# Kernel tuning notes

Hardware: AMD Instinct MI355X
Metric: run time of the kernel (lower is better)

The kernel has to match this reference:

```python
import jax, jax.numpy as jnp
import numpy as np

B, S, E = 8, 1024, 768
H, D = 12, 64
SCALE = 1.0 / np.sqrt(D).astype(np.float32)


def setup_inputs() -> dict:
    key = jax.random.key(0)
    ks = jax.random.split(key, 12)
    s = 0.02
    inp = {
        "queries": jax.random.normal(ks[0], (B, S, E), jnp.float32),
        "keys": jax.random.normal(ks[1], (B, S, E), jnp.float32),
        "values": jax.random.normal(ks[2], (B, S, E), jnp.float32),
        # causal mask for decoder attention (True = keep)
        "attn_mask": jnp.tril(jnp.ones((S, S), dtype=bool)),
        # per-head projections stacked over the head axis
        "Wq": jax.random.normal(ks[3], (H, E, D), jnp.float32) * s,
        "bq": jax.random.normal(ks[4], (H, D), jnp.float32) * s,
        "Wk": jax.random.normal(ks[5], (H, E, D), jnp.float32) * s,
        "bk": jax.random.normal(ks[6], (H, D), jnp.float32) * s,
        "Wv": jax.random.normal(ks[7], (H, E, D), jnp.float32) * s,
        "bv": jax.random.normal(ks[8], (H, D), jnp.float32) * s,
        "Wo": jax.random.normal(ks[9], (H * D, E), jnp.float32) * s,
        "bo": jax.random.normal(ks[10], (E,), jnp.float32) * s,
    }
    return inp


def reference(queries, keys, values, attn_mask, Wq, bq, Wk, bk, Wv, bv, Wo, bo):
    # Batched equivalent of the per-head Python loop (eval mode: dropout is identity).
    Q = jnp.einsum("bse,hed->bhsd", queries, Wq) + bq[:, None, :]   # [B,H,S,D]
    K = jnp.einsum("bte,hed->bhtd", keys, Wk) + bk[:, None, :]
    V = jnp.einsum("bte,hed->bhtd", values, Wv) + bv[:, None, :]
    scores = jnp.einsum("bhsd,bhtd->bhst", Q, K) * SCALE             # [B,H,S,S]
    scores = jnp.where(attn_mask, scores, -jnp.inf)
    weights = jax.nn.softmax(scores, axis=-1)
    heads = jnp.einsum("bhst,bhtd->bhsd", weights, V)                # [B,H,S,D]
    concat = heads.transpose(0, 2, 1, 3).reshape(queries.shape[0], queries.shape[1], -1)  # [B,S,H*D]
    return concat @ Wo + bo                                          # [B,S,E]
```

## Files before the change

kernel.cpp:

```cpp
#include <hip/hip_runtime.h>

#define B_ 8
#define S_ 1024
#define E_ 768
#define H_ 12
#define D_ 64
#define HD_ 768
#define SCALE_ 0.125f

typedef short s16x8 __attribute__((ext_vector_type(8)));
typedef float f32x4 __attribute__((ext_vector_type(4)));
typedef unsigned int u32x4 __attribute__((ext_vector_type(4)));
typedef unsigned short u16;
typedef unsigned int u32;

#define MFMA16(a,b,c) __builtin_amdgcn_mfma_f32_16x16x32_bf16((a),(b),(c),0,0,0)

__device__ __forceinline__ u16 f2bf(float x){
  unsigned u = __float_as_uint(x);
  u += 0x7fffu + ((u >> 16) & 1u);
  return (u16)(u >> 16);
}

__device__ __forceinline__ u32 pack2(float a, float b){
  return (u32)f2bf(a) | ((u32)f2bf(b) << 16);
}

__device__ __forceinline__ u32 cvtpk(float a, float b){
  u32 r;
  asm("v_cvt_pk_bf16_f32 %0, %1, %2" : "=v"(r) : "v"(a), "v"(b));
  return r;
}

#define GLOAD_LDS16(srcp, dstp)                                                        \
  __builtin_amdgcn_global_load_lds(                                                    \
      (const __attribute__((address_space(1))) u32*)(srcp),                            \
      (__attribute__((address_space(3))) u32*)(dstp), 16, 0, 0)

__global__ void prep_weights(const float* __restrict__ Wq, const float* __restrict__ Wk,
                             const float* __restrict__ Wv, const float* __restrict__ Wo,
                             u16* __restrict__ Wt_qkv, u16* __restrict__ Wot) {
  __shared__ float t[64][65];
  const int bid = blockIdx.x;
  const int tid = threadIdx.x;
  const int c = tid & 63;
  const int rg = tid >> 6;
  if (bid < 432) {
    int z = bid / 144, r = bid % 144, h = r / 12, et = r % 12;
    const float* W = (z == 0) ? Wq : ((z == 1) ? Wk : Wv);
    const float* src = W + (size_t)(h * E_ + et * 64) * D_;
#pragma unroll
    for (int p = 0; p < 16; ++p)
      t[rg + 4 * p][c] = src[(rg + 4 * p) * D_ + c];
    __syncthreads();
    u16* dst = Wt_qkv + (size_t)z * HD_ * E_ + (h * 64) * E_ + et * 64;
#pragma unroll
    for (int p = 0; p < 16; ++p) {
      int d = rg + 4 * p;
      dst[d * E_ + c] = f2bf(t[c][d]);
    }
  } else {
    int r = bid - 432; int kt = r / 12, nt = r % 12;
    const float* src = Wo + (size_t)(kt * 64) * E_ + nt * 64;
#pragma unroll
    for (int p = 0; p < 16; ++p)
      t[rg + 4 * p][c] = src[(rg + 4 * p) * E_ + c];
    __syncthreads();
    u16* dst = Wot + (size_t)(nt * 64) * HD_ + kt * 64;
#pragma unroll
    for (int p = 0; p < 16; ++p) {
      int nl = rg + 4 * p;
      dst[nl * HD_ + c] = f2bf(t[c][nl]);
    }
  }
}

__launch_bounds__(256)
__global__ void qkv_gemm(const float* __restrict__ qin, const float* __restrict__ kin,
                         const float* __restrict__ vin, const u16* __restrict__ Wt_qkv,
                         const float* __restrict__ bq, const float* __restrict__ bk,
                         const float* __restrict__ bv, u16* __restrict__ Qbf,
                         u16* __restrict__ Kbf, u16* __restrict__ Vt) {
  __shared__ __align__(16) float Asf[128 * 64];
  __shared__ __align__(16) u16  Bs[128 * 64];
  const int tid = threadIdx.x;
  const int lane = tid & 63;
  const int w = tid >> 6;
  const int wr = w >> 1, wc = w & 1;
  const int m0 = blockIdx.x * 128;
  const int n0 = blockIdx.y * 128;
  const int z  = blockIdx.z;
  const float* in = (z == 0) ? qin : ((z == 1) ? kin : vin);
  const u16* Wt = Wt_qkv + z * (HD_ * E_);
  const float* bias = (z == 0) ? bq : ((z == 1) ? bk : bv);

  f32x4 acc[4][4];
#pragma unroll
  for (int i = 0; i < 4; ++i)
#pragma unroll
    for (int j = 0; j < 4; ++j) acc[i][j] = (f32x4){0.f, 0.f, 0.f, 0.f};

  const int g = lane >> 4;
  const int l15 = lane & 15;
  const int arow = lane >> 4;
  const int ach  = lane & 15;
  const int brow = lane >> 3;
  const int bch  = lane & 7;

  for (int kt = 0; kt < E_ / 64; ++kt) {
    __syncthreads();
#pragma unroll
    for (int i = 0; i < 8; ++i) {
      int row = i * 16 + w * 4 + arow;
      GLOAD_LDS16(in + (size_t)(m0 + row) * E_ + kt * 64 + ((ach ^ (row & 15)) << 2),
                  &Asf[(i * 16 + w * 4) * 64]);
    }
#pragma unroll
    for (int j = 0; j < 4; ++j) {
      int row = j * 32 + w * 8 + brow;
      GLOAD_LDS16(Wt + (n0 + row) * E_ + kt * 64 + ((bch ^ (row & 7)) << 3),
                  &Bs[(j * 32 + w * 8) * 64]);
    }
    __syncthreads();
#pragma unroll
    for (int kk = 0; kk < 2; ++kk) {
      const int kc = kk * 4 + g;
      s16x8 af[4], bfr[4];
#pragma unroll
      for (int i = 0; i < 4; ++i) {
        int row = wr * 64 + i * 16 + l15;
        const float* rp = Asf + row * 64;
        f32x4 lo = *(const f32x4*)(rp + ((( 2 * kc )     ^ (row & 15)) << 2));
        f32x4 hi = *(const f32x4*)(rp + ((( 2 * kc + 1 ) ^ (row & 15)) << 2));
        u32x4 q;
        q[0] = cvtpk(lo[0], lo[1]);
        q[1] = cvtpk(lo[2], lo[3]);
        q[2] = cvtpk(hi[0], hi[1]);
        q[3] = cvtpk(hi[2], hi[3]);
        af[i] = __builtin_bit_cast(s16x8, q);
      }
#pragma unroll
      for (int j = 0; j < 4; ++j) {
        int row = wc * 64 + j * 16 + l15;
        bfr[j] = *(const s16x8*)(Bs + row * 64 + ((kc ^ (row & 7)) << 3));
      }
#pragma unroll
      for (int i = 0; i < 4; ++i)
#pragma unroll
        for (int j = 0; j < 4; ++j) acc[i][j] = MFMA16(af[i], bfr[j], acc[i][j]);
    }
  }
#pragma unroll
  for (int j = 0; j < 4; ++j) {
    int ng = n0 + wc * 64 + j * 16 + l15;
    float bvv = bias[ng];
    int h = ng >> 6, d = ng & 63;
#pragma unroll
    for (int i = 0; i < 4; ++i) {
#pragma unroll
      for (int r = 0; r < 4; ++r) {
        int m = m0 + wr * 64 + i * 16 + g * 4 + r;
        float v = acc[i][j][r] + bvv;
        int bb = m >> 10, s = m & 1023;
        if (z == 0) {
          v *= SCALE_;
          Qbf[((bb * H_ + h) * S_ + s) * D_ + d] = f2bf(v);
        } else if (z == 1) {
          Kbf[((bb * H_ + h) * S_ + s) * D_ + d] = f2bf(v);
        } else {
          Vt[((bb * H_ + h) * D_ + d) * S_ + s] = f2bf(v);
        }
      }
    }
  }
}

__launch_bounds__(256)
__global__ void attn_kernel(const u16* __restrict__ Qbf, const u16* __restrict__ Kbf,
                            const u16* __restrict__ Vt, u16* __restrict__ concat) {
  __shared__ __align__(16) u16 Ks[2][64 * 64];
  __shared__ __align__(16) u16 Vs[2][64 * 64];
  __shared__ __align__(16) u16 Ps[4][2][16 * 64];
  const int tid = threadIdx.x;
  const int lane = tid & 63;
  const int w = tid >> 6;
  const int l15 = lane & 15;
  const int g = lane >> 4;
  const int qb = blockIdx.x & 7;
  const int bh = blockIdx.x >> 3;
  const int h = bh % H_;
  const int b = bh / H_;
  const u16* Qb = Qbf + (b * H_ + h) * S_ * D_;
  const u16* Kb = Kbf + (b * H_ + h) * S_ * D_;
  const u16* Vb = Vt  + (b * H_ + h) * D_ * S_;
  const int q0 = qb * 128;
  const int qrow_base = q0 + w * 32;

  s16x8 qf[2][2];
#pragma unroll
  for (int qg = 0; qg < 2; ++qg)
#pragma unroll
    for (int kk = 0; kk < 2; ++kk)
      qf[qg][kk] = *(const s16x8*)(Qb + (qrow_base + qg * 16 + l15) * D_ + kk * 32 + g * 8);

  f32x4 o[2][4];
#pragma unroll
  for (int qg = 0; qg < 2; ++qg)
#pragma unroll
    for (int dc = 0; dc < 4; ++dc) o[qg][dc] = (f32x4){0.f, 0.f, 0.f, 0.f};
  float lsum[2] = {0.f, 0.f};

  const int nt = 2 * qb + 2;
  const int srow = lane >> 3;
  const int schunk = lane & 7;

#define STAGE(tt, bsel)                                                              \
  {                                                                                  \
    const int t0s = (tt) * 64;                                                       \
    _Pragma("unroll")                                                                \
    for (int j = 0; j < 2; ++j) {                                                    \
      int row = w * 16 + j * 8 + srow;                                               \
      GLOAD_LDS16(Kb + (t0s + row) * D_ + ((schunk ^ (row & 7)) << 3),               \
                  &Ks[bsel][(w * 16 + j * 8) * 64]);                                 \
      GLOAD_LDS16(Vb + row * S_ + t0s + ((schunk ^ (row & 7)) << 3),                 \
                  &Vs[bsel][(w * 16 + j * 8) * 64]);                                 \
    }                                                                                \
  }

  STAGE(0, 0);
  __syncthreads();
  int cur = 0;
  for (int t = 0; t < nt; ++t) {
    if (t + 1 < nt) STAGE(t + 1, cur ^ 1);
    const int t0 = t * 64;
    const u16* Kl = Ks[cur];
    const u16* Vl = Vs[cur];
    f32x4 st[2][4];
#pragma unroll
    for (int qg = 0; qg < 2; ++qg)
#pragma unroll
      for (int c = 0; c < 4; ++c) st[qg][c] = (f32x4){0.f, 0.f, 0.f, 0.f};
#pragma unroll
    for (int kk = 0; kk < 2; ++kk) {
      s16x8 kf[4];
#pragma unroll
      for (int c = 0; c < 4; ++c) {
        int row = 16 * c + l15;
        kf[c] = *(const s16x8*)(Kl + row * 64 + ((((kk << 2) + g) ^ (row & 7)) << 3));
      }
#pragma unroll
      for (int qg = 0; qg < 2; ++qg)
#pragma unroll
        for (int c = 0; c < 4; ++c) st[qg][c] = MFMA16(kf[c], qf[qg][kk], st[qg][c]);
    }
#pragma unroll
    for (int qg = 0; qg < 2; ++qg) {
      const int qmin = qrow_base + qg * 16;
      if (t0 > qmin + 15) continue;
      const bool needmask = (t0 + 63 > qmin);
      const int qv = qmin + l15;
      u16* Pq = Ps[w][qg];
      float lacc = 0.f;
#pragma unroll
      for (int c = 0; c < 4; ++c) {
        float p[4];
#pragma unroll
        for (int r = 0; r < 4; ++r) {
          float s = st[qg][c][r];
          if (needmask && (t0 + 16 * c + 4 * g + r > qv)) s = -1e30f;
          p[r] = __expf(s);
          lacc += p[r];
        }
        int chunk = (2 * c + (g >> 1)) ^ (l15 & 7);
        *(uint2*)(Pq + l15 * 64 + (chunk << 3) + ((g & 1) << 2)) =
            make_uint2(pack2(p[0], p[1]), pack2(p[2], p[3]));
      }
      lsum[qg] += lacc;
    }
    asm volatile("s_waitcnt lgkmcnt(0)" ::: "memory");
    __builtin_amdgcn_sched_barrier(0);
#pragma unroll
    for (int kk = 0; kk < 2; ++kk) {
      s16x8 vf[4];
#pragma unroll
      for (int dc = 0; dc < 4; ++dc) {
        int row = 16 * dc + l15;
        vf[dc] = *(const s16x8*)(Vl + row * 64 + ((((kk << 2) + g) ^ (row & 7)) << 3));
      }
#pragma unroll
      for (int qg = 0; qg < 2; ++qg) {
        if (t0 > qrow_base + qg * 16 + 15) continue;
        s16x8 pf = *(const s16x8*)(Ps[w][qg] + l15 * 64 +
                                   ((((kk << 2) + g) ^ (l15 & 7)) << 3));
#pragma unroll
        for (int dc = 0; dc < 4; ++dc) o[qg][dc] = MFMA16(vf[dc], pf, o[qg][dc]);
      }
    }
    __syncthreads();
    cur ^= 1;
  }
#pragma unroll
  for (int qg = 0; qg < 2; ++qg) {
    float l = lsum[qg];
    l += __shfl_xor(l, 16);
    l += __shfl_xor(l, 32);
    float linv = 1.0f / l;
    int q = qrow_base + qg * 16 + l15;
    u16* Cr = concat + (b * S_ + q) * HD_ + h * D_;
#pragma unroll
    for (int dc = 0; dc < 4; ++dc) {
      *(uint2*)(Cr + dc * 16 + g * 4) =
          make_uint2(pack2(o[qg][dc][0] * linv, o[qg][dc][1] * linv),
                     pack2(o[qg][dc][2] * linv, o[qg][dc][3] * linv));
    }
  }
#undef STAGE
}

__launch_bounds__(256)
__global__ void out_gemm(const u16* __restrict__ concat, const u16* __restrict__ Wot,
                         const float* __restrict__ bo, float* __restrict__ out) {
  __shared__ __align__(16) u16 As[128 * 64];
  __shared__ __align__(16) u16 Bs[128 * 64];
  const int tid = threadIdx.x;
  const int lane = tid & 63;
  const int w = tid >> 6;
  const int wr = w >> 1, wc = w & 1;
  const int m0 = blockIdx.x * 128;
  const int n0 = blockIdx.y * 128;
  f32x4 acc[4][4];
#pragma unroll
  for (int i = 0; i < 4; ++i)
#pragma unroll
    for (int j = 0; j < 4; ++j) acc[i][j] = (f32x4){0.f, 0.f, 0.f, 0.f};
  const int g = lane >> 4;
  const int l15 = lane & 15;
  const int srow = lane >> 3;
  const int sch  = (lane & 7) ^ srow;

  for (int kt = 0; kt < HD_ / 64; ++kt) {
    __syncthreads();
#pragma unroll
    for (int i = 0; i < 4; ++i) {
      int row = i * 32 + w * 8 + srow;
      GLOAD_LDS16(concat + (m0 + row) * HD_ + kt * 64 + sch * 8, &As[(i * 32 + w * 8) * 64]);
      GLOAD_LDS16(Wot    + (n0 + row) * HD_ + kt * 64 + sch * 8, &Bs[(i * 32 + w * 8) * 64]);
    }
    __syncthreads();
#pragma unroll
    for (int kk = 0; kk < 2; ++kk) {
      const int kc = kk * 4 + g;
      s16x8 af[4], bfr[4];
#pragma unroll
      for (int i = 0; i < 4; ++i) {
        int row = wr * 64 + i * 16 + l15;
        af[i] = *(const s16x8*)(As + row * 64 + ((kc ^ (row & 7)) << 3));
      }
#pragma unroll
      for (int j = 0; j < 4; ++j) {
        int row = wc * 64 + j * 16 + l15;
        bfr[j] = *(const s16x8*)(Bs + row * 64 + ((kc ^ (row & 7)) << 3));
      }
#pragma unroll
      for (int i = 0; i < 4; ++i)
#pragma unroll
        for (int j = 0; j < 4; ++j) acc[i][j] = MFMA16(af[i], bfr[j], acc[i][j]);
    }
  }
#pragma unroll
  for (int j = 0; j < 4; ++j) {
    int ng = n0 + wc * 64 + j * 16 + l15;
    float bvv = bo[ng];
#pragma unroll
    for (int i = 0; i < 4; ++i) {
      int mrow = m0 + wr * 64 + i * 16 + g * 4;
#pragma unroll
      for (int r = 0; r < 4; ++r) out[(mrow + r) * E_ + ng] = acc[i][j][r] + bvv;
    }
  }
}

extern "C" void kernel_launch(void* const* d_in, const int* in_sizes, int n_in,
                              void* d_out, int out_size, void* d_ws, size_t ws_size,
                              hipStream_t stream) {
  const float* queries = (const float*)d_in[0];
  const float* keys    = (const float*)d_in[1];
  const float* values  = (const float*)d_in[2];
  const float* Wq = (const float*)d_in[4];
  const float* bq = (const float*)d_in[5];
  const float* Wk = (const float*)d_in[6];
  const float* bk = (const float*)d_in[7];
  const float* Wv = (const float*)d_in[8];
  const float* bv = (const float*)d_in[9];
  const float* Wo = (const float*)d_in[10];
  const float* bo = (const float*)d_in[11];
  float* out = (float*)d_out;

  u16* Wt_qkv = (u16*)d_ws;
  u16* Wot    = Wt_qkv + 3 * HD_ * E_;
  u16* Qbf    = Wot + E_ * HD_;
  u16* Kbf    = Qbf + B_ * H_ * S_ * D_;
  u16* Vt     = Kbf + B_ * H_ * S_ * D_;
  u16* concat = Vt  + B_ * H_ * S_ * D_;

  prep_weights<<<dim3(576), dim3(256), 0, stream>>>(Wq, Wk, Wv, Wo, Wt_qkv, Wot);
  qkv_gemm<<<dim3(64, 6, 3), dim3(256), 0, stream>>>(
      queries, keys, values, Wt_qkv, bq, bk, bv, Qbf, Kbf, Vt);
  attn_kernel<<<dim3(768), dim3(256), 0, stream>>>(Qbf, Kbf, Vt, concat);
  out_gemm<<<dim3(64, 6), dim3(256), 0, stream>>>(concat, Wot, bo, out);
}
```

Measured before the change: 147.8 us.

## Double-buffer QKV GEMM LDS tiles with K=32 stages and async prefetch

Restructures the QKV projection GEMM main loop to use two LDS buffers of K=32 slices. The global-to-LDS load for stage t+2 is issued while stage t is computed, using vmcnt waits and raw barriers in place of full __syncthreads. MFMA priority is raised with s_setprio. This aims to hide global load latency behind matrix math. The cost is more barriers per K and smaller per-stage work, with swizzle patterns rewritten for the 32-wide rows.

```diff
diff --git a/kernel.cpp b/kernel.cpp
--- a/kernel.cpp
+++ b/kernel.cpp
@@ -81,8 +81,8 @@
                          const float* __restrict__ bq, const float* __restrict__ bk,
                          const float* __restrict__ bv, u16* __restrict__ Qbf,
                          u16* __restrict__ Kbf, u16* __restrict__ Vt) {
-  __shared__ __align__(16) float Asf[128 * 64];
-  __shared__ __align__(16) u16  Bs[128 * 64];
+  __shared__ __align__(16) float Asf[2][128 * 32];
+  __shared__ __align__(16) u16  Bs[2][128 * 32];
   const int tid = threadIdx.x;
   const int lane = tid & 63;
   const int w = tid >> 6;
@@ -102,54 +102,76 @@
 
   const int g = lane >> 4;
   const int l15 = lane & 15;
-  const int arow = lane >> 4;
-  const int ach  = lane & 15;
-  const int brow = lane >> 3;
-  const int bch  = lane & 7;
-
-  for (int kt = 0; kt < E_ / 64; ++kt) {
-    __syncthreads();
-#pragma unroll
-    for (int i = 0; i < 8; ++i) {
-      int row = i * 16 + w * 4 + arow;
-      GLOAD_LDS16(in + (size_t)(m0 + row) * E_ + kt * 64 + ((ach ^ (row & 15)) << 2),
-                  &Asf[(i * 16 + w * 4) * 64]);
+  const int aro = lane >> 3;
+  const int schA = (lane & 7) ^ aro;
+  const int bro = lane >> 2;
+  const int schB = (lane & 3) ^ (bro & 3);
+
+#define QSTAGE(kt, bsel)                                                              \
+  {                                                                                   \
+    _Pragma("unroll")                                                                 \
+    for (int i = 0; i < 4; ++i) {                                                     \
+      int row = i * 32 + w * 8 + aro;                                                 \
+      GLOAD_LDS16(in + (size_t)(m0 + row) * E_ + (kt) * 32 + schA * 4,                \
+                  &Asf[bsel][(i * 32 + w * 8) * 32]);                                 \
+    }                                                                                 \
+    _Pragma("unroll")                                                                 \
+    for (int j = 0; j < 2; ++j) {                                                     \
+      int row = j * 64 + w * 16 + bro;                                                \
+      GLOAD_LDS16(Wt + (n0 + row) * E_ + (kt) * 32 + schB * 8,                        \
+                  &Bs[bsel][(j * 64 + w * 16) * 32]);                                 \
+    }                                                                                 \
+  }
+
+  QSTAGE(0, 0);
+  QSTAGE(1, 1);
+  asm volatile("s_waitcnt vmcnt(6)" ::: "memory");
+  __builtin_amdgcn_sched_barrier(0);
+  __builtin_amdgcn_s_barrier();
+  __builtin_amdgcn_sched_barrier(0);
+  for (int t = 0; t < 24; ++t) {
+    const int cur = t & 1;
+    const float* Al = Asf[cur];
+    const u16*   Bl = Bs[cur];
+    s16x8 af[4], bfr[4];
+#pragma unroll
+    for (int i = 0; i < 4; ++i) {
+      int row = wr * 64 + i * 16 + l15;
+      const float* rp = Al + row * 32;
+      f32x4 lo = *(const f32x4*)(rp + (((2 * g)     ^ (row & 7)) << 2));
+      f32x4 hi = *(const f32x4*)(rp + (((2 * g + 1) ^ (row & 7)) << 2));
+      u32x4 q;
+      q[0] = cvtpk(lo[0], lo[1]);
+      q[1] = cvtpk(lo[2], lo[3]);
+      q[2] = cvtpk(hi[0], hi[1]);
+      q[3] = cvtpk(hi[2], hi[3]);
+      af[i] = __builtin_bit_cast(s16x8, q);
     }
 #pragma unroll
     for (int j = 0; j < 4; ++j) {
-      int row = j * 32 + w * 8 + brow;
-      GLOAD_LDS16(Wt + (n0 + row) * E_ + kt * 64 + ((bch ^ (row & 7)) << 3),
-                  &Bs[(j * 32 + w * 8) * 64]);
-    }
-    __syncthreads();
-#pragma unroll
-    for (int kk = 0; kk < 2; ++kk) {
-      const int kc = kk * 4 + g;
-      s16x8 af[4], bfr[4];
-#pragma unroll
-      for (int i = 0; i < 4; ++i) {
-        int row = wr * 64 + i * 16 + l15;
-        const float* rp = Asf + row * 64;
-        f32x4 lo = *(const f32x4*)(rp + ((( 2 * kc )     ^ (row & 15)) << 2));
-        f32x4 hi = *(const f32x4*)(rp + ((( 2 * kc + 1 ) ^ (row & 15)) << 2));
-        u32x4 q;
-        q[0] = cvtpk(lo[0], lo[1]);
-        q[1] = cvtpk(lo[2], lo[3]);
-        q[2] = cvtpk(hi[0], hi[1]);
-        q[3] = cvtpk(hi[2], hi[3]);
-        af[i] = __builtin_bit_cast(s16x8, q);
-      }
-#pragma unroll
-      for (int j = 0; j < 4; ++j) {
-        int row = wc * 64 + j * 16 + l15;
-        bfr[j] = *(const s16x8*)(Bs + row * 64 + ((kc ^ (row & 7)) << 3));
-      }
-#pragma unroll
-      for (int i = 0; i < 4; ++i)
-#pragma unroll
-        for (int j = 0; j < 4; ++j) acc[i][j] = MFMA16(af[i], bfr[j], acc[i][j]);
-    }
-  }
+      int row = wc * 64 + j * 16 + l15;
+      bfr[j] = *(const s16x8*)(Bl + row * 32 + ((g ^ (row & 3)) << 3));
+    }
+    __builtin_amdgcn_s_setprio(1);
+#pragma unroll
+    for (int i = 0; i < 4; ++i)
+#pragma unroll
+      for (int j = 0; j < 4; ++j) acc[i][j] = MFMA16(af[i], bfr[j], acc[i][j]);
+    __builtin_amdgcn_s_setprio(0);
+    if (t < 23) {
+      __builtin_amdgcn_s_barrier();
+      if (t < 22) {
+        QSTAGE(t + 2, cur);
+        asm volatile("s_waitcnt vmcnt(6)" ::: "memory");
+      } else {
+        asm volatile("s_waitcnt vmcnt(0)" ::: "memory");
+      }
+      __builtin_amdgcn_sched_barrier(0);
+      __builtin_amdgcn_s_barrier();
+      __builtin_amdgcn_sched_barrier(0);
+    }
+  }
+#undef QSTAGE
 #pragma unroll
   for (int j = 0; j < 4; ++j) {
     int ng = n0 + wc * 64 + j * 16 + l15;
```

New measurement: 148.9 us. About the same (+0.8%).
